# Optimization experiments

Hardware: AMD Instinct MI355X
Metric: run time of the kernel (lower is better)

The kernel has to match this reference:

```python
import jax, jax.numpy as jnp
import numpy as np


def setup_inputs() -> dict:
    key = jax.random.key(0)
    k1, k2, k3 = jax.random.split(key, 3)
    N, C, H, W, K = 64, 128, 64, 64, 64
    x = jax.random.normal(k1, (N, C, H, W), dtype=jnp.float32)
    conv_w = jax.random.normal(k2, (K, C), dtype=jnp.float32) * 0.05
    centroids = jax.random.uniform(k3, (K, C), dtype=jnp.float32)
    return {"x": x, "conv_w": conv_w, "centroids": centroids}


def reference(x, conv_w, centroids):
    # x: [N, C, H, W]; conv_w: [K, C] (1x1 conv, no bias); centroids: [K, C]
    n, c = x.shape[:2]
    x_flat = x.reshape(n, c, -1)                      # [N, C, S]
    # 1x1 conv == per-pixel linear map, then softmax over clusters
    logits = jnp.einsum('kc,ncs->nks', conv_w, x_flat)  # [N, K, S]
    a = jax.nn.softmax(logits, axis=1)                  # softmax over K
    # VLAD: sum_s a[n,k,s] * (x[n,:,s] - centroid[k])
    #     = (a @ x^T) - (sum_s a) * centroid   -- two batched GEMMs, no [N,K,C,S] blowup
    vlad = jnp.einsum('nks,ncs->nkc', a, x_flat) - a.sum(axis=-1)[..., None] * centroids[None]
    # intra-normalization (L2 per cluster), flatten, global L2
    vlad = vlad / jnp.linalg.norm(vlad, axis=2, keepdims=True)
    vlad = vlad.reshape(n, -1)
    vlad = vlad / jnp.linalg.norm(vlad, axis=1, keepdims=True)
    return vlad
```

## Files before the change

kernel.cpp:

```cpp
#include <hip/hip_runtime.h>


#define Nn 64
#define Cc 128
#define Ss 4096
#define Kk 64
#define TS 64
#define CH 8
#define SB (TS*CH)
#define Pp 8

typedef __attribute__((ext_vector_type(8))) short bf16x8;
typedef __attribute__((ext_vector_type(4))) float f32x4;

__device__ __forceinline__ unsigned f2bf(float f) {
  unsigned u = __float_as_uint(f);
  u = (u + 0x7FFFu + ((u >> 16) & 1u)) >> 16;
  return u;
}

__device__ __forceinline__ void bar_lds() {
  asm volatile("s_waitcnt lgkmcnt(0)\n\ts_barrier" ::: "memory");
}

#define XCS_STR 72
#define AKS_STR 72

__launch_bounds__(256, 2)
__global__ void netvlad_main(const float* __restrict__ x,
                             const float* __restrict__ w,
                             float* __restrict__ vlad,
                             float* __restrict__ asum,
                             int use_atomic)
{
  __shared__ __align__(16) unsigned short x_cs[2][Cc][XCS_STR];
  __shared__ __align__(16) unsigned short a_ks[Kk][AKS_STR];

  const int t   = threadIdx.x;
  const int wv  = t >> 6;
  const int l15 = t & 15;
  const int l4  = (t >> 4) & 3;
  const int n   = blockIdx.y;
  const int sb  = blockIdx.x;
  const size_t xbase = (size_t)n * Cc * Ss;

  bf16x8 wfrag[4][4];
#pragma unroll
  for (int mt = 0; mt < 4; ++mt) {
#pragma unroll
    for (int q = 0; q < 4; ++q) {
      const float* wp = w + (16*mt + l15) * Cc + 32*q + 8*l4;
      float4 a = *(const float4*)wp;
      float4 b = *(const float4*)(wp + 4);
      bf16x8 f;
      f[0] = (short)f2bf(a.x); f[1] = (short)f2bf(a.y);
      f[2] = (short)f2bf(a.z); f[3] = (short)f2bf(a.w);
      f[4] = (short)f2bf(b.x); f[5] = (short)f2bf(b.y);
      f[6] = (short)f2bf(b.z); f[7] = (short)f2bf(b.w);
      wfrag[mt][q] = f;
    }
  }

  f32x4 acc3[4][2];
#pragma unroll
  for (int mt = 0; mt < 4; ++mt)
#pragma unroll
    for (int tc = 0; tc < 2; ++tc) acc3[mt][tc] = (f32x4){0.f,0.f,0.f,0.f};
  float asum_reg[4][4];
#pragma unroll
  for (int mt = 0; mt < 4; ++mt)
#pragma unroll
    for (int r = 0; r < 4; ++r) asum_reg[mt][r] = 0.f;

  const int s4 = 4 * l15;
  const int cb = t >> 4;
  const float* px0 = x + xbase + (size_t)cb * Ss + sb * SB + s4;
  float4 v[8];
#pragma unroll
  for (int it = 0; it < 8; ++it)
    v[it] = *(const float4*)(px0 + (size_t)(16 * it) * Ss);

  for (int ch = 0; ch < CH; ++ch) {
    const int buf = ch & 1;

#pragma unroll
    for (int it = 0; it < 8; ++it) {
      float4 vv = v[it];
      unsigned p0 = f2bf(vv.x) | (f2bf(vv.y) << 16);
      unsigned p1 = f2bf(vv.z) | (f2bf(vv.w) << 16);
      *(int2*)&x_cs[buf][cb + 16*it][s4] = make_int2((int)p0, (int)p1);
    }
    if (ch + 1 < CH) {
      const float* px = px0 + (ch + 1) * TS;
#pragma unroll
      for (int it = 0; it < 8; ++it)
        v[it] = *(const float4*)(px + (size_t)(16 * it) * Ss);
    }
    bar_lds();

    bf16x8 bfr[4];
#pragma unroll
    for (int j = 0; j < 4; ++j) {
      const int c8 = 32*j + 8*l4;
      unsigned short h[8];
#pragma unroll
      for (int i = 0; i < 8; ++i) {
        const int i2 = (i + 2*l4) & 7;
        h[i2] = x_cs[buf][c8 + i2][16*wv + l15];
      }
      bf16x8 f;
#pragma unroll
      for (int i = 0; i < 8; ++i) f[i] = (short)h[i];
      bfr[j] = f;
    }

    f32x4 acc1[4];
#pragma unroll
    for (int mt = 0; mt < 4; ++mt) acc1[mt] = (f32x4){0.f,0.f,0.f,0.f};
#pragma unroll
    for (int q = 0; q < 4; ++q) {
#pragma unroll
      for (int mt = 0; mt < 4; ++mt)
        acc1[mt] = __builtin_amdgcn_mfma_f32_16x16x32_bf16(wfrag[mt][q], bfr[q], acc1[mt], 0, 0, 0);
    }

    float e[4][4];
    float cs = 0.f;
#pragma unroll
    for (int mt = 0; mt < 4; ++mt)
#pragma unroll
      for (int r = 0; r < 4; ++r) {
        float ev = __expf(acc1[mt][r]);
        e[mt][r] = ev;
        cs += ev;
      }
    cs += __shfl_xor(cs, 16, 64);
    cs += __shfl_xor(cs, 32, 64);
    const float inv = 1.0f / cs;
#pragma unroll
    for (int mt = 0; mt < 4; ++mt)
#pragma unroll
      for (int r = 0; r < 4; ++r) {
        float an = e[mt][r] * inv;
        asum_reg[mt][r] += an;
        a_ks[16*mt + 4*l4 + r][16*wv + l15] = (unsigned short)f2bf(an);
      }
    bar_lds();

#pragma unroll
    for (int q2 = 0; q2 < 2; ++q2) {
      bf16x8 afr[4];
#pragma unroll
      for (int mt = 0; mt < 4; ++mt)
        afr[mt] = *(bf16x8*)&a_ks[16*mt + l15][32*q2 + 8*l4];
#pragma unroll
      for (int tc = 0; tc < 2; ++tc) {
        bf16x8 bfx = *(bf16x8*)&x_cs[buf][32*wv + 16*tc + l15][32*q2 + 8*l4];
#pragma unroll
        for (int mt = 0; mt < 4; ++mt)
          acc3[mt][tc] = __builtin_amdgcn_mfma_f32_16x16x32_bf16(afr[mt], bfx, acc3[mt][tc], 0, 0, 0);
      }
    }
  }

  bar_lds();
  float* asml = (float*)a_ks;
#pragma unroll
  for (int mt = 0; mt < 4; ++mt) {
#pragma unroll
    for (int r = 0; r < 4; ++r) {
      float vv = asum_reg[mt][r];
      vv += __shfl_xor(vv, 1, 64);
      vv += __shfl_xor(vv, 2, 64);
      vv += __shfl_xor(vv, 4, 64);
      vv += __shfl_xor(vv, 8, 64);
      if (l15 == 0) asml[wv * Kk + 16*mt + 4*l4 + r] = vv;
    }
  }
  bar_lds();
  if (t < Kk) {
    float s = asml[t] + asml[Kk + t] + asml[2*Kk + t] + asml[3*Kk + t];
    if (use_atomic) atomicAdd(&asum[n * Kk + t], s);
    else            asum[((size_t)sb * Nn + n) * Kk + t] = s;
  }

  if (use_atomic) {
#pragma unroll
    for (int mt = 0; mt < 4; ++mt)
#pragma unroll
      for (int tc = 0; tc < 2; ++tc)
#pragma unroll
        for (int r = 0; r < 4; ++r) {
          const int k = 16*mt + 4*l4 + r;
          const int c = 32*wv + 16*tc + l15;
          atomicAdd(&vlad[((size_t)n * Kk + k) * Cc + c], acc3[mt][tc][r]);
        }
  } else {
    float* vp = vlad + ((size_t)sb * Nn + n) * (Kk * Cc);
#pragma unroll
    for (int mt = 0; mt < 4; ++mt)
#pragma unroll
      for (int tc = 0; tc < 2; ++tc)
#pragma unroll
        for (int r = 0; r < 4; ++r) {
          const int k = 16*mt + 4*l4 + r;
          const int c = 32*wv + 16*tc + l15;
          vp[k * Cc + c] = acc3[mt][tc][r];
        }
  }
}

__global__ void netvlad_epilogue(const float* __restrict__ vlad,
                                 const float* __restrict__ asum,
                                 const float* __restrict__ cent,
                                 float* __restrict__ out,
                                 int nparts)
{
  const int n  = blockIdx.x;
  const int k  = 16*blockIdx.y + (threadIdx.x >> 4);
  const int cq = threadIdx.x & 15;

  float ak = 0.f;
  float4 x0 = make_float4(0.f, 0.f, 0.f, 0.f);
  float4 x1 = make_float4(0.f, 0.f, 0.f, 0.f);
  for (int p = 0; p < nparts; ++p) {
    ak += asum[((size_t)p * Nn + n) * Kk + k];
    const float* vp = vlad + (((size_t)p * Nn + n) * Kk + k) * Cc + 8*cq;
    float4 a0 = *(const float4*)vp;
    float4 a1 = *(const float4*)(vp + 4);
    x0.x += a0.x; x0.y += a0.y; x0.z += a0.z; x0.w += a0.w;
    x1.x += a1.x; x1.y += a1.y; x1.z += a1.z; x1.w += a1.w;
  }

  const size_t cbse = (size_t)k * Cc + 8*cq;
  float4 c0 = *(const float4*)(cent + cbse);
  float4 c1 = *(const float4*)(cent + cbse + 4);
  float4 r0, r1;
  r0.x = x0.x - ak*c0.x; r0.y = x0.y - ak*c0.y; r0.z = x0.z - ak*c0.z; r0.w = x0.w - ak*c0.w;
  r1.x = x1.x - ak*c1.x; r1.y = x1.y - ak*c1.y; r1.z = x1.z - ak*c1.z; r1.w = x1.w - ak*c1.w;
  float ss = r0.x*r0.x + r0.y*r0.y + r0.z*r0.z + r0.w*r0.w
           + r1.x*r1.x + r1.y*r1.y + r1.z*r1.z + r1.w*r1.w;
  ss += __shfl_xor(ss, 1, 64);
  ss += __shfl_xor(ss, 2, 64);
  ss += __shfl_xor(ss, 4, 64);
  ss += __shfl_xor(ss, 8, 64);
  const float rn = rsqrtf(ss) * 0.125f;
  r0.x *= rn; r0.y *= rn; r0.z *= rn; r0.w *= rn;
  r1.x *= rn; r1.y *= rn; r1.z *= rn; r1.w *= rn;
  float* op = out + (size_t)n * (Kk * Cc) + (size_t)k * Cc + 8*cq;
  *(float4*)op = r0;
  *(float4*)(op + 4) = r1;
}

extern "C" void kernel_launch(void* const* d_in, const int* in_sizes, int n_in,
                              void* d_out, int out_size, void* d_ws, size_t ws_size,
                              hipStream_t stream)
{
  const float* x    = (const float*)d_in[0];
  const float* w    = (const float*)d_in[1];
  const float* cent = (const float*)d_in[2];
  float* out = (float*)d_out;

  const size_t vlad_elems_p = (size_t)Pp * Nn * Kk * Cc;
  const size_t asum_elems_p = (size_t)Pp * Nn * Kk;
  const size_t need = (vlad_elems_p + asum_elems_p) * sizeof(float);

  if (ws_size >= need) {
    float* vlad_part = (float*)d_ws;
    float* asum_part = vlad_part + vlad_elems_p;
    netvlad_main<<<dim3(Pp, Nn), 256, 0, stream>>>(x, w, vlad_part, asum_part, 0);
    netvlad_epilogue<<<dim3(Nn, 4), 256, 0, stream>>>(vlad_part, asum_part, cent, out, Pp);
  } else {
    float* vlad = (float*)d_ws;
    float* asum = vlad + (size_t)Nn * Kk * Cc;
    const size_t zbytes = ((size_t)Nn * Kk * Cc + (size_t)Nn * Kk) * sizeof(float);
    hipMemsetAsync(d_ws, 0, zbytes, stream);
    netvlad_main<<<dim3(Pp, Nn), 256, 0, stream>>>(x, w, vlad, asum, 1);
    netvlad_epilogue<<<dim3(Nn, 4), 256, 0, stream>>>(vlad, asum, cent, out, 1);
  }
}
```

Baseline: 210.4 us.

## Fuse centroid subtraction into main kernel and reduce partials via atomics into output

The per-partition workspace write and the epilogue's reduction over partitions are removed. Each block now subtracts asum*centroid itself and atomically adds its partial VLAD straight into the zeroed output, so a lighter norm kernel only has to rescale in place. The grid is also transposed so blocks from the same sample launch apart, which may spread atomic contention. This cuts the workspace round trip (8 partials of 2 MB each) but adds a memset and float atomics whose summation order is non-deterministic.

```diff
diff --git a/kernel.cpp b/kernel.cpp
--- a/kernel.cpp
+++ b/kernel.cpp
@@ -29,9 +29,8 @@
 __launch_bounds__(256, 2)
 __global__ void netvlad_main(const float* __restrict__ x,
                              const float* __restrict__ w,
-                             float* __restrict__ vlad,
-                             float* __restrict__ asum,
-                             int use_atomic)
+                             const float* __restrict__ cent,
+                             float* __restrict__ out)
 {
   __shared__ __align__(16) unsigned short x_cs[2][Cc][XCS_STR];
   __shared__ __align__(16) unsigned short a_ks[Kk][AKS_STR];
@@ -40,8 +39,8 @@
   const int wv  = t >> 6;
   const int l15 = t & 15;
   const int l4  = (t >> 4) & 3;
-  const int n   = blockIdx.y;
-  const int sb  = blockIdx.x;
+  const int n   = blockIdx.x;
+  const int sb  = blockIdx.y;
   const size_t xbase = (size_t)n * Cc * Ss;
 
   bf16x8 wfrag[4][4];
@@ -178,66 +177,36 @@
     }
   }
   bar_lds();
-  if (t < Kk) {
-    float s = asml[t] + asml[Kk + t] + asml[2*Kk + t] + asml[3*Kk + t];
-    if (use_atomic) atomicAdd(&asum[n * Kk + t], s);
-    else            asum[((size_t)sb * Nn + n) * Kk + t] = s;
-  }
-
-  if (use_atomic) {
-#pragma unroll
-    for (int mt = 0; mt < 4; ++mt)
-#pragma unroll
-      for (int tc = 0; tc < 2; ++tc)
-#pragma unroll
-        for (int r = 0; r < 4; ++r) {
-          const int k = 16*mt + 4*l4 + r;
-          const int c = 32*wv + 16*tc + l15;
-          atomicAdd(&vlad[((size_t)n * Kk + k) * Cc + c], acc3[mt][tc][r]);
-        }
-  } else {
-    float* vp = vlad + ((size_t)sb * Nn + n) * (Kk * Cc);
-#pragma unroll
-    for (int mt = 0; mt < 4; ++mt)
-#pragma unroll
-      for (int tc = 0; tc < 2; ++tc)
-#pragma unroll
-        for (int r = 0; r < 4; ++r) {
-          const int k = 16*mt + 4*l4 + r;
-          const int c = 32*wv + 16*tc + l15;
-          vp[k * Cc + c] = acc3[mt][tc][r];
-        }
-  }
-}
-
-__global__ void netvlad_epilogue(const float* __restrict__ vlad,
-                                 const float* __restrict__ asum,
-                                 const float* __restrict__ cent,
-                                 float* __restrict__ out,
-                                 int nparts)
+  if (t < Kk)
+    asml[t] = asml[t] + asml[Kk + t] + asml[2*Kk + t] + asml[3*Kk + t];
+  bar_lds();
+
+  float* op = out + (size_t)n * (Kk * Cc);
+#pragma unroll
+  for (int mt = 0; mt < 4; ++mt) {
+#pragma unroll
+    for (int r = 0; r < 4; ++r) {
+      const int k = 16*mt + 4*l4 + r;
+      const float ak = asml[k];
+#pragma unroll
+      for (int tc = 0; tc < 2; ++tc) {
+        const int c = 32*wv + 16*tc + l15;
+        const float cv = cent[k * Cc + c];
+        unsafeAtomicAdd(op + k * Cc + c, acc3[mt][tc][r] - ak * cv);
+      }
+    }
+  }
+}
+
+__global__ void netvlad_norm(float* __restrict__ out)
 {
   const int n  = blockIdx.x;
   const int k  = 16*blockIdx.y + (threadIdx.x >> 4);
   const int cq = threadIdx.x & 15;
 
-  float ak = 0.f;
-  float4 x0 = make_float4(0.f, 0.f, 0.f, 0.f);
-  float4 x1 = make_float4(0.f, 0.f, 0.f, 0.f);
-  for (int p = 0; p < nparts; ++p) {
-    ak += asum[((size_t)p * Nn + n) * Kk + k];
-    const float* vp = vlad + (((size_t)p * Nn + n) * Kk + k) * Cc + 8*cq;
-    float4 a0 = *(const float4*)vp;
-    float4 a1 = *(const float4*)(vp + 4);
-    x0.x += a0.x; x0.y += a0.y; x0.z += a0.z; x0.w += a0.w;
-    x1.x += a1.x; x1.y += a1.y; x1.z += a1.z; x1.w += a1.w;
-  }
-
-  const size_t cbse = (size_t)k * Cc + 8*cq;
-  float4 c0 = *(const float4*)(cent + cbse);
-  float4 c1 = *(const float4*)(cent + cbse + 4);
-  float4 r0, r1;
-  r0.x = x0.x - ak*c0.x; r0.y = x0.y - ak*c0.y; r0.z = x0.z - ak*c0.z; r0.w = x0.w - ak*c0.w;
-  r1.x = x1.x - ak*c1.x; r1.y = x1.y - ak*c1.y; r1.z = x1.z - ak*c1.z; r1.w = x1.w - ak*c1.w;
+  float* op = out + (size_t)n * (Kk * Cc) + (size_t)k * Cc + 8*cq;
+  float4 r0 = *(const float4*)op;
+  float4 r1 = *(const float4*)(op + 4);
   float ss = r0.x*r0.x + r0.y*r0.y + r0.z*r0.z + r0.w*r0.w
            + r1.x*r1.x + r1.y*r1.y + r1.z*r1.z + r1.w*r1.w;
   ss += __shfl_xor(ss, 1, 64);
@@ -247,7 +216,6 @@
   const float rn = rsqrtf(ss) * 0.125f;
   r0.x *= rn; r0.y *= rn; r0.z *= rn; r0.w *= rn;
   r1.x *= rn; r1.y *= rn; r1.z *= rn; r1.w *= rn;
-  float* op = out + (size_t)n * (Kk * Cc) + (size_t)k * Cc + 8*cq;
   *(float4*)op = r0;
   *(float4*)(op + 4) = r1;
 }
@@ -256,26 +224,13 @@
                               void* d_out, int out_size, void* d_ws, size_t ws_size,
                               hipStream_t stream)
 {
+  (void)d_ws; (void)ws_size;
   const float* x    = (const float*)d_in[0];
   const float* w    = (const float*)d_in[1];
   const float* cent = (const float*)d_in[2];
   float* out = (float*)d_out;
 
-  const size_t vlad_elems_p = (size_t)Pp * Nn * Kk * Cc;
-  const size_t asum_elems_p = (size_t)Pp * Nn * Kk;
-  const size_t need = (vlad_elems_p + asum_elems_p) * sizeof(float);
-
-  if (ws_size >= need) {
-    float* vlad_part = (float*)d_ws;
-    float* asum_part = vlad_part + vlad_elems_p;
-    netvlad_main<<<dim3(Pp, Nn), 256, 0, stream>>>(x, w, vlad_part, asum_part, 0);
-    netvlad_epilogue<<<dim3(Nn, 4), 256, 0, stream>>>(vlad_part, asum_part, cent, out, Pp);
-  } else {
-    float* vlad = (float*)d_ws;
-    float* asum = vlad + (size_t)Nn * Kk * Cc;
-    const size_t zbytes = ((size_t)Nn * Kk * Cc + (size_t)Nn * Kk) * sizeof(float);
-    hipMemsetAsync(d_ws, 0, zbytes, stream);
-    netvlad_main<<<dim3(Pp, Nn), 256, 0, stream>>>(x, w, vlad, asum, 1);
-    netvlad_epilogue<<<dim3(Nn, 4), 256, 0, stream>>>(vlad, asum, cent, out, 1);
-  }
-}
+  hipMemsetAsync(out, 0, (size_t)Nn * Kk * Cc * sizeof(float), stream);
+  netvlad_main<<<dim3(Nn, Pp), 256, 0, stream>>>(x, w, cent, out);
+  netvlad_norm<<<dim3(Nn, 4), 256, 0, stream>>>(out);
+}
```

New measurement: 222.2 us. +5.6%, slower.
